# Optimization experiments

Measured on AMD Instinct MI355X. Metric: run time of the kernel, lower is better.

Reference implementation:

```python
import jax, jax.numpy as jnp
import numpy as np
from jax import lax

NCLASSES = 3
NMS_PRE = 100
NMS_THR = 0.01
SCORE_THR = 0.1
MAX_NUM = 50
H, W = 248, 216
BS = 16


def make_anchors():
    # Faithful to Anchors(ranges, sizes, rotations) in __init__.
    z0s = np.array([-0.6, -0.6, -1.78], np.float32)
    sizes = np.array([[0.6, 0.8, 1.73], [0.6, 1.76, 1.73], [1.6, 3.9, 1.56]], np.float32)
    rotations = np.array([0.0, 1.57], np.float32)
    x = (np.arange(W, dtype=np.float32) + 0.5) * (69.12 / W)
    y = (np.arange(H, dtype=np.float32) + 0.5) * (79.36 / H) - 39.68
    yy, xx = np.meshgrid(y, x, indexing='ij')  # (H, W)
    anchors = np.zeros((H, W, 3, 2, 7), np.float32)
    for c in range(3):
        for r in range(2):
            anchors[:, :, c, r, 0] = xx
            anchors[:, :, c, r, 1] = yy
            anchors[:, :, c, r, 2] = z0s[c]
            anchors[:, :, c, r, 3:6] = sizes[c]
            anchors[:, :, c, r, 6] = rotations[r]
    return jnp.asarray(anchors)


def setup_inputs() -> dict:
    key = jax.random.key(0)
    k1, k2, k3 = jax.random.split(key, 3)
    return {
        'bbox_cls_pred': jax.random.normal(k1, (BS, 18, H, W), jnp.float32),
        'bbox_pred': jax.random.normal(k2, (BS, 42, H, W), jnp.float32) * 0.1,
        'bbox_dir_cls_pred': jax.random.normal(k3, (BS, 12, H, W), jnp.float32),
        'anchors': make_anchors(),
    }


def limit_period(val, offset=1.0, period=np.pi):
    return val - jnp.floor(val / period + offset) * period


def anchors2bboxes(anchors, deltas):
    xa, ya, za, wa, la, ha, ra = [anchors[:, i] for i in range(7)]
    dx, dy, dz, dw, dl, dh, dr = [deltas[:, i] for i in range(7)]
    da = jnp.sqrt(wa * wa + la * la)
    x = dx * da + xa
    y = dy * da + ya
    z = dz * ha + za + ha * 0.5
    w = wa * jnp.exp(dw)
    l = la * jnp.exp(dl)
    h = ha * jnp.exp(dh)
    z = z - h * 0.5
    theta = ra + dr
    return jnp.stack([x, y, z, w, l, h, theta], axis=-1)


def nms_keep(boxes2d, scores, valid, thresh):
    # Greedy NMS over fixed NMS_PRE boxes; invalid boxes never kept / never suppress.
    n = scores.shape[0]
    order = jnp.argsort(-jnp.where(valid, scores, -jnp.inf))
    b = boxes2d[order]
    v = valid[order]
    area = (b[:, 2] - b[:, 0]) * (b[:, 3] - b[:, 1])
    x1 = jnp.maximum(b[:, None, 0], b[None, :, 0])
    y1 = jnp.maximum(b[:, None, 1], b[None, :, 1])
    x2 = jnp.minimum(b[:, None, 2], b[None, :, 2])
    y2 = jnp.minimum(b[:, None, 3], b[None, :, 3])
    inter = jnp.maximum(x2 - x1, 0.0) * jnp.maximum(y2 - y1, 0.0)
    iou = inter / (area[:, None] + area[None, :] - inter + 1e-8)
    idx = jnp.arange(n)
    def body(i, keep):
        sup = (iou[i] > thresh) & (idx > i) & keep[i]
        return keep & ~sup
    keep = lax.fori_loop(0, n, body, v)
    return jnp.zeros(n, bool).at[order].set(keep)


def process_single(cls_pred, box_pred, dir_pred, anchors):
    # cls_pred (18,H,W), box_pred (42,H,W), dir_pred (12,H,W), anchors (H,W,3,2,7)
    cls = jnp.transpose(cls_pred, (1, 2, 0)).reshape(-1, NCLASSES)
    box = jnp.transpose(box_pred, (1, 2, 0)).reshape(-1, 7)
    dirp = jnp.transpose(dir_pred, (1, 2, 0)).reshape(-1, 2)
    anc = anchors.reshape(-1, 7)
    cls = jax.nn.sigmoid(cls)
    dir_cls = jnp.argmax(dirp, axis=1)
    _, inds = lax.top_k(jnp.max(cls, axis=1), NMS_PRE)
    cls = cls[inds]
    box = box[inds]
    dir_cls = dir_cls[inds]
    anc = anc[inds]
    bboxes = anchors2bboxes(anc, box)  # (NMS_PRE, 7): x,y,z,w,l,h,theta
    xy = bboxes[:, :2]
    wl = bboxes[:, 3:5]
    boxes2d = jnp.concatenate([xy - wl / 2, xy + wl / 2], axis=-1)
    # Torch code detaches theta through limit_period; dir term is constant.
    theta = lax.stop_gradient(limit_period(bboxes[:, 6])) + (1.0 - dir_cls.astype(bboxes.dtype)) * np.pi
    bboxes = bboxes.at[:, 6].set(theta)
    keeps = []
    for c in range(NCLASSES):
        sc = cls[:, c]
        valid = sc > SCORE_THR
        keeps.append(nms_keep(boxes2d, sc, valid, NMS_THR) & valid)
    keep = jnp.stack(keeps)            # (3, NMS_PRE)
    scores_all = cls.T                 # (3, NMS_PRE)
    flat = jnp.where(keep, scores_all, -1.0).reshape(-1)
    final_scores, fi = lax.top_k(flat, MAX_NUM)
    sel = fi % NMS_PRE
    labels = fi // NMS_PRE
    out_bboxes = bboxes[sel]
    mask = final_scores > 0.0
    return out_bboxes, labels, final_scores, mask


def reference(bbox_cls_pred, bbox_pred, bbox_dir_cls_pred, anchors):
    f = jax.vmap(process_single, in_axes=(0, 0, 0, None))
    return f(bbox_cls_pred, bbox_pred, bbox_dir_cls_pred, anchors)
```

## Files before the change

kernel.cpp:

```cpp
#include <hip/hip_runtime.h>
#include <cstdint>

#pragma clang fp contract(off)

#define HH 248
#define WW 216
#define HW (HH*WW)
#define NROW (6*HW)
#define BATCH 16
#define NPRE 100
#define MAXNUM 50
#define NB 4096
#define CAP 2048
#define SBLK 53
#define PIF 3.14159274101257324f

#define CNT_OFF  0
#define TB_OFF   64
#define KEYS_OFF 128
#define SH_OFF   (KEYS_OFF + BATCH*CAP*8)

__device__ __forceinline__ float sigmoidf_ref(float x) {
    if (x >= 0.0f) {
        return 1.0f / (1.0f + expf(-x));
    } else {
        float e = expf(x);
        return e / (1.0f + e);
    }
}

__device__ __forceinline__ unsigned bucket_of(unsigned bits) {
    unsigned b = (bits >= 0x3F000000u) ? (2048u + ((bits - 0x3F000000u) >> 12))
                                       : (bits >> 19);
    return (b > (unsigned)(NB - 1)) ? (unsigned)(NB - 1) : b;
}

__global__ __launch_bounds__(256) void k_score(const float* __restrict__ cls,
                                               unsigned short* __restrict__ subhist,
                                               unsigned* __restrict__ cnt) {
    int t = threadIdx.x, blk = blockIdx.x, b = blockIdx.y;
    __shared__ unsigned hist[NB];
    for (int i = t; i < NB; i += 256) hist[i] = 0;
    if (blk == 0 && t == 0) cnt[b] = 0;
    __syncthreads();

    int cell0 = blk * 1024 + t * 4;
    if (cell0 < HW) {
        const float* p = cls + (size_t)b * 18 * HW;
        for (int a = 0; a < 6; ++a) {
            float4 l0 = *(const float4*)(p + (size_t)(a*3+0)*HW + cell0);
            float4 l1 = *(const float4*)(p + (size_t)(a*3+1)*HW + cell0);
            float4 l2 = *(const float4*)(p + (size_t)(a*3+2)*HW + cell0);
            unsigned b0 = __float_as_uint(sigmoidf_ref(fmaxf(l0.x, fmaxf(l1.x, l2.x))));
            unsigned b1 = __float_as_uint(sigmoidf_ref(fmaxf(l0.y, fmaxf(l1.y, l2.y))));
            unsigned b2 = __float_as_uint(sigmoidf_ref(fmaxf(l0.z, fmaxf(l1.z, l2.z))));
            unsigned b3 = __float_as_uint(sigmoidf_ref(fmaxf(l0.w, fmaxf(l1.w, l2.w))));
            atomicAdd(&hist[bucket_of(b0)], 1u);
            atomicAdd(&hist[bucket_of(b1)], 1u);
            atomicAdd(&hist[bucket_of(b2)], 1u);
            atomicAdd(&hist[bucket_of(b3)], 1u);
        }
    }
    __syncthreads();
    unsigned short* sh = subhist + (size_t)(b * SBLK + blk) * NB;
    for (int i = t; i < NB; i += 256) sh[i] = (unsigned short)hist[i];
}

__global__ __launch_bounds__(256) void k_reduce(const unsigned short* __restrict__ subhist,
                                                unsigned* __restrict__ tbo) {
    int b = blockIdx.x, t = threadIdx.x;
    __shared__ unsigned h[NB];
    __shared__ unsigned csum[256];
    const unsigned short* base = subhist + (size_t)b * SBLK * NB;
    for (int j = t; j < NB; j += 256) {
        unsigned s = 0;
        for (int k = 0; k < SBLK; ++k) s += base[(size_t)k * NB + j];
        h[j] = s;
    }
    __syncthreads();
    unsigned cs = 0;
    for (int q = 0; q < 16; ++q) cs += h[t * 16 + q];
    csum[t] = cs;
    __syncthreads();
    if (t == 0) {
        unsigned cum = 0;
        int r = 0;
        for (int u = 255; u >= 0; --u) {
            if (cum + csum[u] >= NPRE) {
                unsigned c2 = cum;
                for (int k2 = (u + 1) * 16 - 1; k2 >= u * 16; --k2) {
                    c2 += h[k2];
                    if (c2 >= NPRE) { r = k2; break; }
                }
                break;
            }
            cum += csum[u];
        }
        tbo[b] = (unsigned)r;
    }
}

__global__ __launch_bounds__(256) void k_collect(const float* __restrict__ cls,
                                                 const unsigned* __restrict__ tbo,
                                                 unsigned* __restrict__ cnt,
                                                 unsigned long long* __restrict__ keys) {
    int t = threadIdx.x, blk = blockIdx.x, b = blockIdx.y;
    int cell0 = blk * 1024 + t * 4;
    if (cell0 >= HW) return;
    unsigned tb = tbo[b];
    const float* p = cls + (size_t)b * 18 * HW;
    for (int a = 0; a < 6; ++a) {
        float4 l0 = *(const float4*)(p + (size_t)(a*3+0)*HW + cell0);
        float4 l1 = *(const float4*)(p + (size_t)(a*3+1)*HW + cell0);
        float4 l2 = *(const float4*)(p + (size_t)(a*3+2)*HW + cell0);
        unsigned bs[4];
        bs[0] = __float_as_uint(sigmoidf_ref(fmaxf(l0.x, fmaxf(l1.x, l2.x))));
        bs[1] = __float_as_uint(sigmoidf_ref(fmaxf(l0.y, fmaxf(l1.y, l2.y))));
        bs[2] = __float_as_uint(sigmoidf_ref(fmaxf(l0.z, fmaxf(l1.z, l2.z))));
        bs[3] = __float_as_uint(sigmoidf_ref(fmaxf(l0.w, fmaxf(l1.w, l2.w))));
        for (int e = 0; e < 4; ++e) {
            unsigned bits = bs[e];
            if (bucket_of(bits) >= tb) {
                unsigned pos = atomicAdd(&cnt[b], 1u);
                if (pos < CAP) {
                    unsigned row = (unsigned)((cell0 + e) * 6 + a);
                    keys[(size_t)b * CAP + pos] =
                        ((unsigned long long)bits << 32) |
                        (unsigned long long)(0xFFFFFFFFu - row);
                }
            }
        }
    }
}

__global__ __launch_bounds__(256) void k_final(
    const float* __restrict__ cls, const float* __restrict__ box,
    const float* __restrict__ dir, const float* __restrict__ anc,
    const unsigned* __restrict__ cnt, const unsigned long long* __restrict__ keys,
    float* __restrict__ out) {
    int b = blockIdx.x, t = threadIdx.x;

    __shared__ unsigned long long keyS[CAP];
    __shared__ int   selRow[NPRE];
    __shared__ float bb[NPRE][7];
    __shared__ float b2d[NPRE][4];
    __shared__ float areaS[NPRE];
    __shared__ float clsS[3][NPRE];
    __shared__ float svalS[3][NPRE];
    __shared__ int   ordS[3][NPRE];
    __shared__ int   rankS[3][NPRE];
    __shared__ unsigned keepInit[3][4];
    __shared__ unsigned long long maskS[3][NPRE][2];
    __shared__ unsigned long long keepBits[3][2];
    __shared__ float flatS[3*NPRE];

    unsigned cn = cnt[b];
    int M = (cn < (unsigned)CAP) ? (int)cn : CAP;
    for (int i = t; i < M; i += 256)
        keyS[i] = keys[(size_t)b * CAP + i];
    __syncthreads();

    for (int i = t; i < M; i += 256) {
        unsigned long long k = keyS[i];
        int r = 0;
        for (int j = 0; j < M; ++j) r += (keyS[j] > k);
        if (r < NPRE) selRow[r] = (int)(0xFFFFFFFFu - (unsigned)(k & 0xFFFFFFFFull));
    }
    __syncthreads();

    if (t < NPRE) {
        int row = selRow[t];
        int a = row % 6;
        int cell = row / 6;
        const float* cb = cls + (size_t)b * 18 * HW + cell;
        clsS[0][t] = sigmoidf_ref(cb[(size_t)(a*3+0)*HW]);
        clsS[1][t] = sigmoidf_ref(cb[(size_t)(a*3+1)*HW]);
        clsS[2][t] = sigmoidf_ref(cb[(size_t)(a*3+2)*HW]);
        const float* db = dir + (size_t)b * 12 * HW + cell;
        float d0 = db[(size_t)(a*2+0)*HW];
        float d1 = db[(size_t)(a*2+1)*HW];
        int dircls = (d1 > d0) ? 1 : 0;
        const float* pb = box + (size_t)b * 42 * HW + cell;
        float dx = pb[(size_t)(a*7+0)*HW], dy = pb[(size_t)(a*7+1)*HW], dz = pb[(size_t)(a*7+2)*HW];
        float dw = pb[(size_t)(a*7+3)*HW], dl = pb[(size_t)(a*7+4)*HW], dh = pb[(size_t)(a*7+5)*HW];
        float dr = pb[(size_t)(a*7+6)*HW];
        const float* ab = anc + (size_t)row * 7;
        float xa = ab[0], ya = ab[1], za = ab[2];
        float wa = ab[3], la = ab[4], ha = ab[5], ra = ab[6];
        float da = sqrtf(wa*wa + la*la);
        float x = dx*da + xa;
        float y = dy*da + ya;
        float z = dz*ha + za + ha*0.5f;
        float wv = wa*expf(dw);
        float lv = la*expf(dl);
        float hv = ha*expf(dh);
        z = z - hv*0.5f;
        float th0 = ra + dr;
        float lim = th0 - floorf(th0/PIF + 1.0f)*PIF;
        float theta = lim + (1.0f - (float)dircls)*PIF;
        bb[t][0]=x; bb[t][1]=y; bb[t][2]=z; bb[t][3]=wv; bb[t][4]=lv; bb[t][5]=hv; bb[t][6]=theta;
        b2d[t][0] = x - wv*0.5f;
        b2d[t][1] = y - lv*0.5f;
        b2d[t][2] = x + wv*0.5f;
        b2d[t][3] = y + lv*0.5f;
        areaS[t] = (b2d[t][2]-b2d[t][0]) * (b2d[t][3]-b2d[t][1]);
    }
    if (t < 12) keepInit[t/4][t%4] = 0u;
    __syncthreads();

    for (int w = t; w < 3*NPRE; w += 256) {
        int c = w / NPRE, p = w % NPRE;
        float sc = clsS[c][p];
        svalS[c][p] = (sc > 0.1f) ? sc : -INFINITY;
    }
    __syncthreads();

    for (int w = t; w < 3*NPRE; w += 256) {
        int c = w / NPRE, p = w % NPRE;
        float v = svalS[c][p];
        int r = 0;
        for (int j = 0; j < NPRE; ++j) {
            float vj = svalS[c][j];
            if (vj > v || (vj == v && j < p)) ++r;
        }
        ordS[c][r] = p;
        rankS[c][p] = r;
        if (v != -INFINITY) atomicOr(&keepInit[c][r >> 5], 1u << (r & 31));
    }
    __syncthreads();

    for (int w = t; w < 3*NPRE; w += 256) {
        int c = w / NPRE, i = w % NPRE;
        int pi = ordS[c][i];
        unsigned long long m0 = 0ULL, m1 = 0ULL;
        float ax1 = b2d[pi][0], ay1 = b2d[pi][1], ax2 = b2d[pi][2], ay2 = b2d[pi][3];
        float ai = areaS[pi];
        for (int j = i + 1; j < NPRE; ++j) {
            int pj = ordS[c][j];
            float x1 = fmaxf(ax1, b2d[pj][0]);
            float y1 = fmaxf(ay1, b2d[pj][1]);
            float x2 = fminf(ax2, b2d[pj][2]);
            float y2 = fminf(ay2, b2d[pj][3]);
            float inter = fmaxf(x2 - x1, 0.0f) * fmaxf(y2 - y1, 0.0f);
            float iou = inter / (ai + areaS[pj] - inter + 1e-8f);
            if (iou > 0.01f) {
                if (j < 64) m0 |= (1ULL << j);
                else        m1 |= (1ULL << (j - 64));
            }
        }
        maskS[c][i][0] = m0;
        maskS[c][i][1] = m1;
    }
    __syncthreads();

    if (t < 3) {
        int c = t;
        unsigned long long k0 = (unsigned long long)keepInit[c][0] |
                                ((unsigned long long)keepInit[c][1] << 32);
        unsigned long long k1 = (unsigned long long)keepInit[c][2] |
                                ((unsigned long long)keepInit[c][3] << 32);
        for (int i = 0; i < NPRE; ++i) {
            unsigned long long bit = (i < 64) ? (k0 >> i) : (k1 >> (i - 64));
            if (bit & 1ULL) {
                k0 &= ~maskS[c][i][0];
                k1 &= ~maskS[c][i][1];
            }
        }
        keepBits[c][0] = k0;
        keepBits[c][1] = k1;
    }
    __syncthreads();

    for (int w = t; w < 3*NPRE; w += 256) {
        int c = w / NPRE, p = w % NPRE;
        int r = rankS[c][p];
        unsigned long long bit = (r < 64) ? (keepBits[c][0] >> r) : (keepBits[c][1] >> (r - 64));
        flatS[w] = (bit & 1ULL) ? clsS[c][p] : -1.0f;
    }
    __syncthreads();

    for (int i = t; i < 3*NPRE; i += 256) {
        float vi = flatS[i];
        int r2 = 0;
        for (int j = 0; j < 3*NPRE; ++j) {
            float vj = flatS[j];
            if (vj > vi || (vj == vi && j < i)) ++r2;
        }
        if (r2 < MAXNUM) {
            int p = i % NPRE;
            int lab = i / NPRE;
            int o = b * MAXNUM + r2;
            float* ob = out + (size_t)o * 7;
            for (int j = 0; j < 7; ++j) ob[j] = bb[p][j];
            out[BATCH*MAXNUM*7 + o] = (float)lab;
            out[BATCH*MAXNUM*8 + o] = vi;
            out[BATCH*MAXNUM*9 + o] = (vi > 0.0f) ? 1.0f : 0.0f;
        }
    }
}

extern "C" void kernel_launch(void* const* d_in, const int* in_sizes, int n_in,
                              void* d_out, int out_size, void* d_ws, size_t ws_size,
                              hipStream_t stream) {
    const float* cls = (const float*)d_in[0];
    const float* box = (const float*)d_in[1];
    const float* dir = (const float*)d_in[2];
    const float* anc = (const float*)d_in[3];
    float* out = (float*)d_out;
    char* ws = (char*)d_ws;

    unsigned* cnt = (unsigned*)(ws + CNT_OFF);
    unsigned* tb  = (unsigned*)(ws + TB_OFF);
    unsigned long long* keys = (unsigned long long*)(ws + KEYS_OFF);
    unsigned short* subhist  = (unsigned short*)(ws + SH_OFF);

    dim3 g(SBLK, BATCH);
    k_score  <<<g, 256, 0, stream>>>(cls, subhist, cnt);
    k_reduce <<<BATCH, 256, 0, stream>>>(subhist, tb);
    k_collect<<<g, 256, 0, stream>>>(cls, tb, cnt, keys);
    k_final  <<<BATCH, 256, 0, stream>>>(cls, box, dir, anc, cnt, keys, out);
}
```

Before: 327.1 us.

## Fuse candidate collection into histogram pass with fixed-threshold speculative keys

```diff
diff --git a/kernel.cpp b/kernel.cpp
--- a/kernel.cpp
+++ b/kernel.cpp
@@ -10,15 +10,17 @@
 #define BATCH 16
 #define NPRE 100
 #define MAXNUM 50
-#define NB 4096
+#define NB 2048
 #define CAP 2048
 #define SBLK 53
+#define K0 64
 #define PIF 3.14159274101257324f
 
-#define CNT_OFF  0
-#define TB_OFF   64
-#define KEYS_OFF 128
-#define SH_OFF   (KEYS_OFF + BATCH*CAP*8)
+#define T0BKT 1966u
+
+#define CNTB_OFF 0
+#define KEYS_OFF 3584
+#define SH_OFF   (KEYS_OFF + BATCH*SBLK*K0*8)
 
 __device__ __forceinline__ float sigmoidf_ref(float x) {
     if (x >= 0.0f) {
@@ -30,23 +32,40 @@
 }
 
 __device__ __forceinline__ unsigned bucket_of(unsigned bits) {
-    unsigned b = (bits >= 0x3F000000u) ? (2048u + ((bits - 0x3F000000u) >> 12))
-                                       : (bits >> 19);
+    unsigned b = (bits >= 0x3F000000u) ? (1024u + ((bits - 0x3F000000u) >> 13))
+                                       : (bits >> 20);
     return (b > (unsigned)(NB - 1)) ? (unsigned)(NB - 1) : b;
+}
+
+__device__ __forceinline__ void emit_one(unsigned bits, unsigned row,
+                                         unsigned* hist, unsigned* lcnt,
+                                         unsigned long long* kseg) {
+    unsigned bk = bucket_of(bits);
+    atomicAdd(&hist[bk], 1u);
+    if (bk >= T0BKT) {
+        unsigned pos = atomicAdd(lcnt, 1u);
+        if (pos < (unsigned)K0)
+            kseg[pos] = ((unsigned long long)bits << 32) |
+                        (unsigned long long)(0xFFFFFFFFu - row);
+    }
 }
 
 __global__ __launch_bounds__(256) void k_score(const float* __restrict__ cls,
                                                unsigned short* __restrict__ subhist,
-                                               unsigned* __restrict__ cnt) {
+                                               unsigned* __restrict__ cntB,
+                                               unsigned long long* __restrict__ keys) {
     int t = threadIdx.x, blk = blockIdx.x, b = blockIdx.y;
     __shared__ unsigned hist[NB];
+    __shared__ unsigned lcnt;
     for (int i = t; i < NB; i += 256) hist[i] = 0;
-    if (blk == 0 && t == 0) cnt[b] = 0;
-    __syncthreads();
-
+    if (t == 0) lcnt = 0;
+    __syncthreads();
+
+    unsigned long long* kseg = keys + (size_t)(b * SBLK + blk) * K0;
     int cell0 = blk * 1024 + t * 4;
     if (cell0 < HW) {
         const float* p = cls + (size_t)b * 18 * HW;
+        #pragma unroll
         for (int a = 0; a < 6; ++a) {
             float4 l0 = *(const float4*)(p + (size_t)(a*3+0)*HW + cell0);
             float4 l1 = *(const float4*)(p + (size_t)(a*3+1)*HW + cell0);
@@ -55,88 +74,23 @@
             unsigned b1 = __float_as_uint(sigmoidf_ref(fmaxf(l0.y, fmaxf(l1.y, l2.y))));
             unsigned b2 = __float_as_uint(sigmoidf_ref(fmaxf(l0.z, fmaxf(l1.z, l2.z))));
             unsigned b3 = __float_as_uint(sigmoidf_ref(fmaxf(l0.w, fmaxf(l1.w, l2.w))));
-            atomicAdd(&hist[bucket_of(b0)], 1u);
-            atomicAdd(&hist[bucket_of(b1)], 1u);
-            atomicAdd(&hist[bucket_of(b2)], 1u);
-            atomicAdd(&hist[bucket_of(b3)], 1u);
+            emit_one(b0, (unsigned)((cell0+0)*6 + a), hist, &lcnt, kseg);
+            emit_one(b1, (unsigned)((cell0+1)*6 + a), hist, &lcnt, kseg);
+            emit_one(b2, (unsigned)((cell0+2)*6 + a), hist, &lcnt, kseg);
+            emit_one(b3, (unsigned)((cell0+3)*6 + a), hist, &lcnt, kseg);
         }
     }
     __syncthreads();
     unsigned short* sh = subhist + (size_t)(b * SBLK + blk) * NB;
     for (int i = t; i < NB; i += 256) sh[i] = (unsigned short)hist[i];
-}
-
-__global__ __launch_bounds__(256) void k_reduce(const unsigned short* __restrict__ subhist,
-                                                unsigned* __restrict__ tbo) {
-    int b = blockIdx.x, t = threadIdx.x;
-    __shared__ unsigned h[NB];
-    __shared__ unsigned csum[256];
-    const unsigned short* base = subhist + (size_t)b * SBLK * NB;
-    for (int j = t; j < NB; j += 256) {
-        unsigned s = 0;
-        for (int k = 0; k < SBLK; ++k) s += base[(size_t)k * NB + j];
-        h[j] = s;
-    }
-    __syncthreads();
-    unsigned cs = 0;
-    for (int q = 0; q < 16; ++q) cs += h[t * 16 + q];
-    csum[t] = cs;
-    __syncthreads();
-    if (t == 0) {
-        unsigned cum = 0;
-        int r = 0;
-        for (int u = 255; u >= 0; --u) {
-            if (cum + csum[u] >= NPRE) {
-                unsigned c2 = cum;
-                for (int k2 = (u + 1) * 16 - 1; k2 >= u * 16; --k2) {
-                    c2 += h[k2];
-                    if (c2 >= NPRE) { r = k2; break; }
-                }
-                break;
-            }
-            cum += csum[u];
-        }
-        tbo[b] = (unsigned)r;
-    }
-}
-
-__global__ __launch_bounds__(256) void k_collect(const float* __restrict__ cls,
-                                                 const unsigned* __restrict__ tbo,
-                                                 unsigned* __restrict__ cnt,
-                                                 unsigned long long* __restrict__ keys) {
-    int t = threadIdx.x, blk = blockIdx.x, b = blockIdx.y;
-    int cell0 = blk * 1024 + t * 4;
-    if (cell0 >= HW) return;
-    unsigned tb = tbo[b];
-    const float* p = cls + (size_t)b * 18 * HW;
-    for (int a = 0; a < 6; ++a) {
-        float4 l0 = *(const float4*)(p + (size_t)(a*3+0)*HW + cell0);
-        float4 l1 = *(const float4*)(p + (size_t)(a*3+1)*HW + cell0);
-        float4 l2 = *(const float4*)(p + (size_t)(a*3+2)*HW + cell0);
-        unsigned bs[4];
-        bs[0] = __float_as_uint(sigmoidf_ref(fmaxf(l0.x, fmaxf(l1.x, l2.x))));
-        bs[1] = __float_as_uint(sigmoidf_ref(fmaxf(l0.y, fmaxf(l1.y, l2.y))));
-        bs[2] = __float_as_uint(sigmoidf_ref(fmaxf(l0.z, fmaxf(l1.z, l2.z))));
-        bs[3] = __float_as_uint(sigmoidf_ref(fmaxf(l0.w, fmaxf(l1.w, l2.w))));
-        for (int e = 0; e < 4; ++e) {
-            unsigned bits = bs[e];
-            if (bucket_of(bits) >= tb) {
-                unsigned pos = atomicAdd(&cnt[b], 1u);
-                if (pos < CAP) {
-                    unsigned row = (unsigned)((cell0 + e) * 6 + a);
-                    keys[(size_t)b * CAP + pos] =
-                        ((unsigned long long)bits << 32) |
-                        (unsigned long long)(0xFFFFFFFFu - row);
-                }
-            }
-        }
-    }
+    if (t == 0) cntB[b * SBLK + blk] = lcnt;
 }
 
 __global__ __launch_bounds__(256) void k_final(
     const float* __restrict__ cls, const float* __restrict__ box,
     const float* __restrict__ dir, const float* __restrict__ anc,
-    const unsigned* __restrict__ cnt, const unsigned long long* __restrict__ keys,
+    const unsigned* __restrict__ cntB, const unsigned long long* __restrict__ keys,
+    const unsigned short* __restrict__ subhist,
     float* __restrict__ out) {
     int b = blockIdx.x, t = threadIdx.x;
 
@@ -153,11 +107,80 @@
     __shared__ unsigned long long maskS[3][NPRE][2];
     __shared__ unsigned long long keepBits[3][2];
     __shared__ float flatS[3*NPRE];
-
-    unsigned cn = cnt[b];
-    int M = (cn < (unsigned)CAP) ? (int)cn : CAP;
-    for (int i = t; i < M; i += 256)
-        keyS[i] = keys[(size_t)b * CAP + i];
+    __shared__ unsigned hq[256];
+    __shared__ int  pref[SBLK + 1];
+    __shared__ int  tbS;
+    __shared__ unsigned cumS;
+    __shared__ int  safeS;
+    __shared__ unsigned lcntF;
+
+    if (t == 0) { tbS = -1; cumS = 0; }
+    __syncthreads();
+    {
+        const unsigned short* base = subhist + (size_t)b * SBLK * NB;
+        for (int c0 = NB - 256; c0 >= 0; c0 -= 256) {
+            unsigned s = 0;
+            #pragma unroll
+            for (int k = 0; k < SBLK; ++k) s += base[(size_t)k * NB + (c0 + t)];
+            hq[t] = s;
+            __syncthreads();
+            if (t == 0) {
+                unsigned cum = cumS;
+                for (int j = 255; j >= 0; --j) {
+                    cum += hq[j];
+                    if (cum >= NPRE) { tbS = c0 + j; break; }
+                }
+                cumS = cum;
+            }
+            __syncthreads();
+            if (tbS >= 0) break;
+        }
+    }
+    int tb = (tbS < 0) ? 0 : tbS;
+
+    if (t == 0) {
+        int ok = (tb >= (int)T0BKT) ? 1 : 0;
+        int s = 0;
+        for (int k = 0; k < SBLK; ++k) {
+            unsigned c = cntB[b * SBLK + k];
+            if (c > (unsigned)K0) ok = 0;
+            pref[k] = s;
+            s += (int)((c < (unsigned)K0) ? c : (unsigned)K0);
+        }
+        pref[SBLK] = s;
+        if (s > CAP || s < NPRE) ok = 0;
+        safeS = ok;
+        lcntF = 0;
+    }
+    __syncthreads();
+
+    int M;
+    if (safeS) {
+        for (int k = 0; k < SBLK; ++k) {
+            int base0 = pref[k], c = pref[k + 1] - pref[k];
+            for (int i = t; i < c; i += 256)
+                keyS[base0 + i] = keys[(size_t)(b * SBLK + k) * K0 + i];
+        }
+        M = pref[SBLK];
+    } else {
+        const float* p = cls + (size_t)b * 18 * HW;
+        for (int cell = t; cell < HW; cell += 256) {
+            for (int a = 0; a < 6; ++a) {
+                float v0 = p[(size_t)(a*3+0)*HW + cell];
+                float v1 = p[(size_t)(a*3+1)*HW + cell];
+                float v2 = p[(size_t)(a*3+2)*HW + cell];
+                unsigned bits = __float_as_uint(sigmoidf_ref(fmaxf(v0, fmaxf(v1, v2))));
+                if (bucket_of(bits) >= (unsigned)tb) {
+                    unsigned pos = atomicAdd(&lcntF, 1u);
+                    if (pos < (unsigned)CAP)
+                        keyS[pos] = ((unsigned long long)bits << 32) |
+                                    (unsigned long long)(0xFFFFFFFFu - (unsigned)(cell*6 + a));
+                }
+            }
+        }
+        __syncthreads();
+        M = (lcntF < (unsigned)CAP) ? (int)lcntF : CAP;
+    }
     __syncthreads();
 
     for (int i = t; i < M; i += 256) {
@@ -309,14 +332,11 @@
     float* out = (float*)d_out;
     char* ws = (char*)d_ws;
 
-    unsigned* cnt = (unsigned*)(ws + CNT_OFF);
-    unsigned* tb  = (unsigned*)(ws + TB_OFF);
+    unsigned* cntB = (unsigned*)(ws + CNTB_OFF);
     unsigned long long* keys = (unsigned long long*)(ws + KEYS_OFF);
     unsigned short* subhist  = (unsigned short*)(ws + SH_OFF);
 
     dim3 g(SBLK, BATCH);
-    k_score  <<<g, 256, 0, stream>>>(cls, subhist, cnt);
-    k_reduce <<<BATCH, 256, 0, stream>>>(subhist, tb);
-    k_collect<<<g, 256, 0, stream>>>(cls, tb, cnt, keys);
-    k_final  <<<BATCH, 256, 0, stream>>>(cls, box, dir, anc, cnt, keys, out);
-}
+    k_score<<<g, 256, 0, stream>>>(cls, subhist, cntB, keys);
+    k_final<<<BATCH, 256, 0, stream>>>(cls, box, dir, anc, cntB, keys, subhist, out);
+}
```

After: 343.1 us. 1.05x slower.
